# Performance work log

Hardware: AMD Instinct MI355X
Metric: run time of the kernel (lower is better)

The kernel has to match this reference:

```python
import jax, jax.numpy as jnp
import numpy as np

N = 1_000_000
D = 128
NUM_CLASSES = 1000


def setup_inputs() -> dict:
    key = jax.random.key(0)
    k1, k2 = jax.random.split(key)
    embeddings = jax.random.normal(k1, (N, D), dtype=jnp.float32)
    labels = jax.random.randint(k2, (N,), 0, NUM_CLASSES, dtype=jnp.int64)
    return {"embeddings": embeddings, "labels": labels}


def reference(embeddings, labels):
    # Per-class mean via one-pass segment sums (equivalent to the torch
    # per-unique-label masked-mean loop, since all classes are present).
    sums = jax.ops.segment_sum(embeddings, labels, num_segments=NUM_CLASSES)  # [C, D]
    counts = jax.ops.segment_sum(
        jnp.ones((embeddings.shape[0],), dtype=embeddings.dtype), labels,
        num_segments=NUM_CLASSES)  # [C]
    class_means = sums / counts[:, None]  # [C, D]
    # torch.var default is unbiased (ddof=1)
    variance = jnp.var(class_means, axis=0, ddof=1).mean()
    return -variance
```

## Files before the change

### kernel.cpp

```cpp
#include <hip/hip_runtime.h>
#include <stdint.h>

#define NROWS 1000000
#define DDIM  128
#define NCLS  1000
#define BUCKET 2048

typedef float f4 __attribute__((ext_vector_type(4)));

#define WS_CURSOR 0
#define WS_SORTED 1024
#define WS_GMEAN  2100000
#define WS_VARD   2228000

__global__ __launch_bounds__(256) void init_kernel(int* __restrict__ cursor) {
    int i = blockIdx.x * 256 + threadIdx.x;
    if (i < NCLS) cursor[i] = i * BUCKET;
}

__global__ __launch_bounds__(256) void scatter_kernel(const int* __restrict__ labels,
                                                      int* __restrict__ cursor,
                                                      int* __restrict__ sorted_idx) {
    for (int r = blockIdx.x * 256 + threadIdx.x; r < NROWS; r += 1024 * 256) {
        int lbl = __builtin_nontemporal_load(&labels[r]);
        int pos = atomicAdd(&cursor[lbl], 1);
        sorted_idx[pos] = r;
    }
}

__global__ __launch_bounds__(512, 4) void gather_sum_kernel(
        const float* __restrict__ emb, const int* __restrict__ cursor,
        const int* __restrict__ sorted_idx, float* __restrict__ gmean) {
    const f4* emb4 = (const f4*)emb;
    const int c    = blockIdx.x;
    const int w    = threadIdx.x >> 6;
    const int lane = threadIdx.x & 63;
    const int half = lane >> 5;
    const int q    = lane & 31;

    const int base = c * BUCKET;
    const int m    = cursor[c] - base;
    const int lo   = base + (int)(((long long)m * w) >> 3);
    const int hi   = base + (int)(((long long)m * (w + 1)) >> 3);

    f4 acc = {0.0f, 0.0f, 0.0f, 0.0f};
    int i = lo;
    int idx = (i + 64 <= hi) ? sorted_idx[i + lane] : 0;
    for (; i + 64 <= hi; i += 64) {
        int idx_next = (i + 128 <= hi) ? sorted_idx[i + 64 + lane] : 0;
        #pragma unroll
        for (int jj = 0; jj < 64; jj += 16) {
            f4 vv[8];
            #pragma unroll
            for (int u = 0; u < 8; u++) {
                int r = __shfl(idx, jj + 2 * u + half);
                vv[u] = __builtin_nontemporal_load(&emb4[(size_t)r * 32 + q]);
            }
            #pragma unroll
            for (int u = 0; u < 8; u++) acc += vv[u];
        }
        idx = idx_next;
    }
    int n = hi - i;
    if (n > 0) {
        int tidx = sorted_idx[i + (lane < n ? lane : n - 1)];
        for (int j = 0; j < n; j += 2) {
            if (j + half < n) {
                int r = __shfl(tidx, j + half);
                acc += __builtin_nontemporal_load(&emb4[(size_t)r * 32 + q]);
            }
        }
    }

    __shared__ float red[16 * DDIM];
    f4* red4 = (f4*)red;
    red4[(w * 2 + half) * 32 + q] = acc;
    __syncthreads();
    if (threadIdx.x < DDIM) {
        float s = 0.0f;
        #pragma unroll
        for (int k = 0; k < 16; k++) s += red[k * DDIM + threadIdx.x];
        gmean[c * DDIM + threadIdx.x] = (m > 0) ? (s / (float)m) : 0.0f;
    }
}

__global__ __launch_bounds__(256) void var_kernel(const float* __restrict__ gmean,
                                                  float* __restrict__ var_d) {
    const int d = blockIdx.x;
    float s1 = 0.0f, s2 = 0.0f;
    for (int c = threadIdx.x; c < NCLS; c += 256) {
        float mv = gmean[c * DDIM + d];
        s1 += mv;
        s2 += mv * mv;
    }
    #pragma unroll
    for (int off = 32; off; off >>= 1) {
        s1 += __shfl_down(s1, off);
        s2 += __shfl_down(s2, off);
    }
    __shared__ float p1[4], p2[4];
    int wave = threadIdx.x >> 6, lane = threadIdx.x & 63;
    if (lane == 0) { p1[wave] = s1; p2[wave] = s2; }
    __syncthreads();
    if (threadIdx.x == 0) {
        float t1 = p1[0] + p1[1] + p1[2] + p1[3];
        float t2 = p2[0] + p2[1] + p2[2] + p2[3];
        var_d[d] = (t2 - t1 * t1 / (float)NCLS) / (float)(NCLS - 1);
    }
}

__global__ __launch_bounds__(64) void final_kernel(const float* __restrict__ var_d,
                                                   float* __restrict__ out) {
    float s = var_d[threadIdx.x] + var_d[threadIdx.x + 64];
    #pragma unroll
    for (int off = 32; off; off >>= 1) s += __shfl_down(s, off);
    if (threadIdx.x == 0) out[0] = -s / (float)DDIM;
}

extern "C" void kernel_launch(void* const* d_in, const int* in_sizes, int n_in,
                              void* d_out, int out_size, void* d_ws, size_t ws_size,
                              hipStream_t stream) {
    const float* emb    = (const float*)d_in[0];
    const int*   labels = (const int*)d_in[1];
    int*   wsi    = (int*)d_ws;
    float* wsf    = (float*)d_ws;
    int*   cursor = wsi + WS_CURSOR;
    int*   sorted = wsi + WS_SORTED;
    float* gmean  = wsf + WS_GMEAN;
    float* var_d  = wsf + WS_VARD;
    float* out    = (float*)d_out;

    hipLaunchKernelGGL(init_kernel, dim3(4), dim3(256), 0, stream, cursor);
    hipLaunchKernelGGL(scatter_kernel, dim3(1024), dim3(256), 0, stream, labels, cursor, sorted);
    hipLaunchKernelGGL(gather_sum_kernel, dim3(NCLS), dim3(512), 0, stream,
                       emb, cursor, sorted, gmean);
    hipLaunchKernelGGL(var_kernel, dim3(DDIM), dim3(256), 0, stream, gmean, var_d);
    hipLaunchKernelGGL(final_kernel, dim3(1), dim3(64), 0, stream, var_d, out);
}
```

Baseline: 833.4 us.

## Replace sort-and-gather with streaming LDS atomic segment-sum over dimension groups

Drops the counting-sort scatter and per-class gather. The new kernel streams embeddings sequentially, and each block accumulates a 16-dimension slice for all classes in shared memory using XOR-swizzled float atomics before flushing to global sums. A separate shared-memory histogram computes the counts. This avoids random row gathers and the index-scatter pass, at the cost of heavy LDS atomic contention, global float atomics, and reading the labels once for every dimension group.

New measurement: 1.194 ms. 1.43x slower.

```diff
diff --git a/kernel.cpp b/kernel.cpp
--- a/kernel.cpp
+++ b/kernel.cpp
@@ -4,92 +4,100 @@
 #define NROWS 1000000
 #define DDIM  128
 #define NCLS  1000
-#define BUCKET 2048
+
+#define DG    8
+#define BPG   64
+#define RPB   ((NROWS + BPG - 1) / BPG)
+#define TPB   1024
 
 typedef float f4 __attribute__((ext_vector_type(4)));
 
-#define WS_CURSOR 0
-#define WS_SORTED 1024
-#define WS_GMEAN  2100000
-#define WS_VARD   2228000
+#define WS_SUMS   0
+#define WS_COUNTS 128000
+#define WS_VARD   129024
 
-__global__ __launch_bounds__(256) void init_kernel(int* __restrict__ cursor) {
-    int i = blockIdx.x * 256 + threadIdx.x;
-    if (i < NCLS) cursor[i] = i * BUCKET;
+__global__ __launch_bounds__(256) void zero_kernel(float* __restrict__ sums,
+                                                   int* __restrict__ counts) {
+    int t = blockIdx.x * 256 + threadIdx.x;
+    if (t < NCLS * DDIM / 4) {
+        f4 z = {0.0f, 0.0f, 0.0f, 0.0f};
+        ((f4*)sums)[t] = z;
+    }
+    int u = t - NCLS * DDIM / 4;
+    if (u >= 0 && u < NCLS) counts[u] = 0;
 }
 
-__global__ __launch_bounds__(256) void scatter_kernel(const int* __restrict__ labels,
-                                                      int* __restrict__ cursor,
-                                                      int* __restrict__ sorted_idx) {
-    for (int r = blockIdx.x * 256 + threadIdx.x; r < NROWS; r += 1024 * 256) {
-        int lbl = __builtin_nontemporal_load(&labels[r]);
-        int pos = atomicAdd(&cursor[lbl], 1);
-        sorted_idx[pos] = r;
+__global__ __launch_bounds__(256) void hist_kernel(const int* __restrict__ labels,
+                                                   int* __restrict__ counts) {
+    __shared__ int h[NCLS];
+    for (int e = threadIdx.x; e < NCLS; e += 256) h[e] = 0;
+    __syncthreads();
+    for (int r = blockIdx.x * 256 + threadIdx.x; r < NROWS; r += 256 * 256)
+        atomicAdd(&h[labels[r]], 1);
+    __syncthreads();
+    for (int e = threadIdx.x; e < NCLS; e += 256) atomicAdd(&counts[e], h[e]);
+}
+
+__global__ __launch_bounds__(TPB) void accum_kernel(const float* __restrict__ emb,
+                                                    const int* __restrict__ labels,
+                                                    float* __restrict__ sums) {
+    __shared__ float part[NCLS * 16];
+    const int g  = blockIdx.x & (DG - 1);
+    const int b  = blockIdx.x / DG;
+    const int q  = threadIdx.x & 3;
+    const int tr = threadIdx.x >> 2;
+
+    f4 zero = {0.0f, 0.0f, 0.0f, 0.0f};
+    f4* part4 = (f4*)part;
+    for (int e = threadIdx.x; e < NCLS * 4; e += TPB) part4[e] = zero;
+    __syncthreads();
+
+    const f4* emb4 = (const f4*)emb;
+    const int r0 = b * RPB;
+    const int r1 = (r0 + RPB < NROWS) ? (r0 + RPB) : NROWS;
+    const int iters = (r1 - r0 + (TPB / 4) - 1) / (TPB / 4);
+
+    int r = r0 + tr;
+    f4 v = zero;
+    int c = 0;
+    bool val = (r < r1);
+    if (val) {
+        v = __builtin_nontemporal_load(&emb4[(size_t)r * 32 + g * 4 + q]);
+        c = labels[r];
+    }
+    for (int it = 0; it < iters; ++it) {
+        const int rn = r + TPB / 4;
+        f4 vn = zero;
+        int cn = 0;
+        const bool valn = (rn < r1);
+        if (valn) {
+            vn = __builtin_nontemporal_load(&emb4[(size_t)rn * 32 + g * 4 + q]);
+            cn = labels[rn];
+        }
+        if (val) {
+            const int m = c & 15, base = c * 16, j0 = q * 4;
+            unsafeAtomicAdd(&part[base + ((j0 + 0) ^ m)], v.x);
+            unsafeAtomicAdd(&part[base + ((j0 + 1) ^ m)], v.y);
+            unsafeAtomicAdd(&part[base + ((j0 + 2) ^ m)], v.z);
+            unsafeAtomicAdd(&part[base + ((j0 + 3) ^ m)], v.w);
+        }
+        v = vn; c = cn; val = valn; r = rn;
+    }
+
+    __syncthreads();
+    for (int e = threadIdx.x; e < NCLS * 16; e += TPB) {
+        const int cc = e >> 4, j = e & 15;
+        unsafeAtomicAdd(&sums[cc * DDIM + g * 16 + j], part[cc * 16 + (j ^ (cc & 15))]);
     }
 }
 
-__global__ __launch_bounds__(512, 4) void gather_sum_kernel(
-        const float* __restrict__ emb, const int* __restrict__ cursor,
-        const int* __restrict__ sorted_idx, float* __restrict__ gmean) {
-    const f4* emb4 = (const f4*)emb;
-    const int c    = blockIdx.x;
-    const int w    = threadIdx.x >> 6;
-    const int lane = threadIdx.x & 63;
-    const int half = lane >> 5;
-    const int q    = lane & 31;
-
-    const int base = c * BUCKET;
-    const int m    = cursor[c] - base;
-    const int lo   = base + (int)(((long long)m * w) >> 3);
-    const int hi   = base + (int)(((long long)m * (w + 1)) >> 3);
-
-    f4 acc = {0.0f, 0.0f, 0.0f, 0.0f};
-    int i = lo;
-    int idx = (i + 64 <= hi) ? sorted_idx[i + lane] : 0;
-    for (; i + 64 <= hi; i += 64) {
-        int idx_next = (i + 128 <= hi) ? sorted_idx[i + 64 + lane] : 0;
-        #pragma unroll
-        for (int jj = 0; jj < 64; jj += 16) {
-            f4 vv[8];
-            #pragma unroll
-            for (int u = 0; u < 8; u++) {
-                int r = __shfl(idx, jj + 2 * u + half);
-                vv[u] = __builtin_nontemporal_load(&emb4[(size_t)r * 32 + q]);
-            }
-            #pragma unroll
-            for (int u = 0; u < 8; u++) acc += vv[u];
-        }
-        idx = idx_next;
-    }
-    int n = hi - i;
-    if (n > 0) {
-        int tidx = sorted_idx[i + (lane < n ? lane : n - 1)];
-        for (int j = 0; j < n; j += 2) {
-            if (j + half < n) {
-                int r = __shfl(tidx, j + half);
-                acc += __builtin_nontemporal_load(&emb4[(size_t)r * 32 + q]);
-            }
-        }
-    }
-
-    __shared__ float red[16 * DDIM];
-    f4* red4 = (f4*)red;
-    red4[(w * 2 + half) * 32 + q] = acc;
-    __syncthreads();
-    if (threadIdx.x < DDIM) {
-        float s = 0.0f;
-        #pragma unroll
-        for (int k = 0; k < 16; k++) s += red[k * DDIM + threadIdx.x];
-        gmean[c * DDIM + threadIdx.x] = (m > 0) ? (s / (float)m) : 0.0f;
-    }
-}
-
-__global__ __launch_bounds__(256) void var_kernel(const float* __restrict__ gmean,
+__global__ __launch_bounds__(256) void var_kernel(const float* __restrict__ sums,
+                                                  const int* __restrict__ counts,
                                                   float* __restrict__ var_d) {
     const int d = blockIdx.x;
     float s1 = 0.0f, s2 = 0.0f;
     for (int c = threadIdx.x; c < NCLS; c += 256) {
-        float mv = gmean[c * DDIM + d];
+        float mv = sums[c * DDIM + d] / (float)counts[c];
         s1 += mv;
         s2 += mv * mv;
     }
@@ -122,18 +130,17 @@
                               hipStream_t stream) {
     const float* emb    = (const float*)d_in[0];
     const int*   labels = (const int*)d_in[1];
+    float* wsf    = (float*)d_ws;
     int*   wsi    = (int*)d_ws;
-    float* wsf    = (float*)d_ws;
-    int*   cursor = wsi + WS_CURSOR;
-    int*   sorted = wsi + WS_SORTED;
-    float* gmean  = wsf + WS_GMEAN;
+    float* sums   = wsf + WS_SUMS;
+    int*   counts = wsi + WS_COUNTS;
     float* var_d  = wsf + WS_VARD;
     float* out    = (float*)d_out;
 
-    hipLaunchKernelGGL(init_kernel, dim3(4), dim3(256), 0, stream, cursor);
-    hipLaunchKernelGGL(scatter_kernel, dim3(1024), dim3(256), 0, stream, labels, cursor, sorted);
-    hipLaunchKernelGGL(gather_sum_kernel, dim3(NCLS), dim3(512), 0, stream,
-                       emb, cursor, sorted, gmean);
-    hipLaunchKernelGGL(var_kernel, dim3(DDIM), dim3(256), 0, stream, gmean, var_d);
+    hipLaunchKernelGGL(zero_kernel, dim3((NCLS * DDIM / 4 + NCLS + 255) / 256), dim3(256),
+                       0, stream, sums, counts);
+    hipLaunchKernelGGL(hist_kernel, dim3(256), dim3(256), 0, stream, labels, counts);
+    hipLaunchKernelGGL(accum_kernel, dim3(DG * BPG), dim3(TPB), 0, stream, emb, labels, sums);
+    hipLaunchKernelGGL(var_kernel, dim3(DDIM), dim3(256), 0, stream, sums, counts, var_d);
     hipLaunchKernelGGL(final_kernel, dim3(1), dim3(64), 0, stream, var_d, out);
 }
```
